# Kernel optimization log

Hardware: AMD Instinct MI355X
Metric: run time of the kernel (lower is better)

## Reference

```python
import jax, jax.numpy as jnp
import numpy as np

VOCAB, EMB = 100000, 128
KERNEL_NUM, SIGMA, EXACT_SIGMA = 21, 0.1, 0.001
OUT_LAYERS = [10, 5]

def _mus_sigmas():
    step = 2.0 / (KERNEL_NUM - 1)
    mus = [1.0, 1.0 - step / 2]
    for i in range(1, KERNEL_NUM - 1):
        mus.append(mus[i] - step)
    mus = list(reversed(mus))  # [-0.95, ..., 0.95, 1.0]
    sigmas = [SIGMA] * (KERNEL_NUM - 1) + [EXACT_SIGMA]
    return mus, sigmas

MUS, SIGMAS = _mus_sigmas()

def setup_inputs() -> dict:
    key = jax.random.key(0)
    ks = jax.random.split(key, 12)
    B, Q, D = 1024, 64, 256
    q1 = jax.random.randint(ks[0], (B, Q), 0, VOCAB, dtype=jnp.int32)
    d1 = jax.random.randint(ks[1], (B, D), 0, VOCAB, dtype=jnp.int32)
    q2 = jax.random.randint(ks[2], (B, Q), 0, VOCAB, dtype=jnp.int32)
    d2 = jax.random.randint(ks[3], (B, D), 0, VOCAB, dtype=jnp.int32)
    emb = jax.random.normal(ks[4], (VOCAB, EMB), dtype=jnp.float32)
    emb = emb.at[0].set(0.0)  # padding_idx=0
    dims = [KERNEL_NUM] + OUT_LAYERS + [1]
    W1 = jax.random.normal(ks[5], (dims[0], dims[1]), dtype=jnp.float32) / np.sqrt(dims[0])
    b1 = jnp.zeros((dims[1],), dtype=jnp.float32)
    W2 = jax.random.normal(ks[6], (dims[1], dims[2]), dtype=jnp.float32) / np.sqrt(dims[1])
    b2 = jnp.zeros((dims[2],), dtype=jnp.float32)
    W3 = jax.random.normal(ks[7], (dims[2], dims[3]), dtype=jnp.float32) / np.sqrt(dims[2])
    b3 = jnp.zeros((dims[3],), dtype=jnp.float32)
    return {"q1": q1, "d1": d1, "q2": q2, "d2": d2, "emb": emb,
            "W1": W1, "b1": b1, "W2": W2, "b2": b2, "W3": W3, "b3": b3}

def _matching_matrix(emb, q_ids, d_ids):
    q = emb[q_ids]  # [B,Q,E]
    d = emb[d_ids]  # [B,D,E]
    qn = q / (jnp.linalg.norm(q, axis=-1, keepdims=True) + 1e-13)
    dn = d / (jnp.linalg.norm(d, axis=-1, keepdims=True) + 1e-13)
    return jnp.einsum('bqe,bde->bqd', qn, dn)  # [B,Q,D]

def _apply_kernels(M):
    KM = []
    for mu, sig in zip(MUS, SIGMAS):
        k = jnp.exp(-(M - mu) ** 2 / (2.0 * sig ** 2))
        KM.append(jnp.log1p(k.sum(axis=-1)).sum(axis=-1))  # [B]
    return jnp.stack(KM, axis=-1)  # [B,21]

def _mlp(x, W1, b1, W2, b2, W3, b3):
    # _get_mlp puts ReLU BEFORE each Linear
    x = jax.nn.relu(x) @ W1 + b1
    x = jax.nn.relu(x) @ W2 + b2
    x = jax.nn.relu(x) @ W3 + b3
    return x  # [B,1]

def _predict(emb, q, d, W1, b1, W2, b2, W3, b3):
    M = _matching_matrix(emb, q, d)
    ko = _apply_kernels(M)
    return _mlp(ko, W1, b1, W2, b2, W3, b3)

def reference(q1, d1, q2, d2, emb, W1, b1, W2, b2, W3, b3):
    l1 = _predict(emb, q1, d1, W1, b1, W2, b2, W3, b3)
    l2 = _predict(emb, q2, d2, W1, b1, W2, b2, W3, b3)
    return jax.nn.sigmoid(l1 - l2)  # [B,1]
```

## Files before the change

### kernel.cpp

```cpp
#include <hip/hip_runtime.h>


typedef __attribute__((ext_vector_type(8))) short bf16x8;
typedef __attribute__((ext_vector_type(4))) float f32x4;
typedef __attribute__((ext_vector_type(2))) float f32x2;

__device__ __forceinline__ unsigned short f2bf(float f) {
    unsigned u = __float_as_uint(f);
    u += 0x7fffu + ((u >> 16) & 1u);
    return (unsigned short)(u >> 16);
}
__device__ __forceinline__ float bf2f(unsigned short h) {
    return __uint_as_float(((unsigned)h) << 16);
}

__global__ __launch_bounds__(256)
void norm_split_kernel(const float* __restrict__ emb,
                       unsigned short* __restrict__ th,
                       unsigned short* __restrict__ tl, int vocab)
{
    const int row = blockIdx.x * 8 + (threadIdx.x >> 5);
    if (row >= vocab) return;
    const int ln = threadIdx.x & 31;
    const float4 v = *reinterpret_cast<const float4*>(emb + (size_t)row * 128 + ln * 4);
    float ss = v.x*v.x + v.y*v.y + v.z*v.z + v.w*v.w;
    #pragma unroll
    for (int m = 16; m >= 1; m >>= 1) ss += __shfl_xor(ss, m);
    const float rn = 1.0f / (sqrtf(ss) + 1e-13f);
    const float f0 = v.x*rn, f1 = v.y*rn, f2 = v.z*rn, f3 = v.w*rn;
    const unsigned short h0 = f2bf(f0), h1 = f2bf(f1), h2 = f2bf(f2), h3 = f2bf(f3);
    const unsigned short g0 = f2bf(f0 - bf2f(h0)), g1 = f2bf(f1 - bf2f(h1));
    const unsigned short g2 = f2bf(f2 - bf2f(h2)), g3 = f2bf(f3 - bf2f(h3));
    const int off = row * 128 + ln * 4;
    *reinterpret_cast<uint2*>(th + off) =
        make_uint2((unsigned)h0 | ((unsigned)h1 << 16), (unsigned)h2 | ((unsigned)h3 << 16));
    *reinterpret_cast<uint2*>(tl + off) =
        make_uint2((unsigned)g0 | ((unsigned)g1 << 16), (unsigned)g2 | ((unsigned)g3 << 16));
}

__device__ __forceinline__ void glds16(const unsigned short* g, unsigned short* l) {
    __builtin_amdgcn_global_load_lds((const __attribute__((address_space(1))) void*)g,
                                     (__attribute__((address_space(3))) void*)l, 16, 0, 0);
}

__device__ __forceinline__ void stage_d16(const unsigned short* __restrict__ th,
                                          const unsigned short* __restrict__ tl,
                                          const int* __restrict__ ids, int base,
                                          unsigned short* __restrict__ dh,
                                          unsigned short* __restrict__ dl,
                                          int w, int l)
{
    const int r   = 4*w + (l >> 4);
    const int id  = ids[base + r];
    const int gsw = ((l & 15) ^ r) << 3;
    glds16(th + (size_t)id * 128 + gsw, dh + 4*w * 128);
    glds16(tl + (size_t)id * 128 + gsw, dl + 4*w * 128);
}

__device__ __forceinline__ void stage_q16(const unsigned short* __restrict__ th,
                                          const unsigned short* __restrict__ tl,
                                          const int* __restrict__ qids,
                                          unsigned short* __restrict__ dh,
                                          unsigned short* __restrict__ dl,
                                          int w, int l)
{
    #pragma unroll
    for (int j = 0; j < 4; j++) {
        const int r   = 4*j + (l >> 4);
        const int id  = qids[16*w + r];
        const int gsw = ((l & 15) ^ r) << 3;
        glds16(th + (size_t)id * 128 + gsw, dh + 4*j * 128);
        glds16(tl + (size_t)id * 128 + gsw, dl + 4*j * 128);
    }
}

#define PKF(a, b, c) __builtin_elementwise_fma((a), (b), (c))

__device__ __forceinline__ void apply_pair(float m0, float m1, f32x2 (&sp)[21]) {
    const f32x2 m2 = {m0, m1};
    const f32x2 dm = m2 - 0.05f;
    const f32x2 ta = (dm * dm) * -72.13475204444817f;
    const f32x2 x2 = m2 * 14.426950408889634f;
    const f32x2 t0 = { __builtin_amdgcn_exp2f(ta[0]), __builtin_amdgcn_exp2f(ta[1]) };
    const f32x2 R  = { __builtin_amdgcn_exp2f(x2[0]), __builtin_amdgcn_exp2f(x2[1]) };
    const f32x2 Ri = { __builtin_amdgcn_exp2f(-x2[0]), __builtin_amdgcn_exp2f(-x2[1]) };
    sp[10] += t0;
    f32x2 tu = t0;
    tu *= R;  sp[11] = PKF(tu, (f32x2)3.6787944117e-1f,  sp[11]);
    tu *= R;  sp[12] = PKF(tu, (f32x2)4.9787068368e-2f,  sp[12]);
    tu *= R;  sp[13] = PKF(tu, (f32x2)2.4787521767e-3f,  sp[13]);
    tu *= R;  sp[14] = PKF(tu, (f32x2)4.5399929762e-5f,  sp[14]);
    tu *= R;  sp[15] = PKF(tu, (f32x2)3.0590232050e-7f,  sp[15]);
    tu *= R;  sp[16] = PKF(tu, (f32x2)7.5825604279e-10f, sp[16]);
    tu *= R;  sp[17] = PKF(tu, (f32x2)6.9144001069e-13f, sp[17]);
    tu *= R;  sp[18] = PKF(tu, (f32x2)2.3195228302e-16f, sp[18]);
    tu *= R;  sp[19] = PKF(tu, (f32x2)2.8625185805e-20f, sp[19]);
    f32x2 td = t0;
    td *= Ri; sp[9] += td;
    td *= Ri; sp[8] = PKF(td, (f32x2)3.6787944117e-1f,  sp[8]);
    td *= Ri; sp[7] = PKF(td, (f32x2)4.9787068368e-2f,  sp[7]);
    td *= Ri; sp[6] = PKF(td, (f32x2)2.4787521767e-3f,  sp[6]);
    td *= Ri; sp[5] = PKF(td, (f32x2)4.5399929762e-5f,  sp[5]);
    td *= Ri; sp[4] = PKF(td, (f32x2)3.0590232050e-7f,  sp[4]);
    td *= Ri; sp[3] = PKF(td, (f32x2)7.5825604279e-10f, sp[3]);
    td *= Ri; sp[2] = PKF(td, (f32x2)6.9144001069e-13f, sp[2]);
    td *= Ri; sp[1] = PKF(td, (f32x2)2.3195228302e-16f, sp[1]);
    td *= Ri; sp[0] = PKF(td, (f32x2)2.8625185805e-20f, sp[0]);
    const f32x2 e  = m2 - 1.0f;
    const f32x2 ea = (e * e) * -721347.5204444817f;
    const f32x2 ex = { __builtin_amdgcn_exp2f(ea[0]), __builtin_amdgcn_exp2f(ea[1]) };
    sp[20] += ex;
}

#define MFMA(a, b, c) __builtin_amdgcn_mfma_f32_16x16x32_bf16((a), (b), (c), 0, 0, 0)

__global__ __launch_bounds__(256, 2)
void knrm_main(const int* __restrict__ q1, const int* __restrict__ d1,
               const int* __restrict__ q2, const int* __restrict__ d2,
               const unsigned short* __restrict__ th, const unsigned short* __restrict__ tl,
               float* __restrict__ kmws)
{
    __shared__ unsigned short bh[4][16*128];
    __shared__ unsigned short bl[4][16*128];
    __shared__ int   sh_ids[256];
    __shared__ float KMpart[4][21];

    const int tid = threadIdx.x;
    const int bb  = blockIdx.x >> 1;
    const int p   = blockIdx.x & 1;
    const int w   = tid >> 6;
    const int l   = tid & 63;
    const int lr  = l & 15;
    const int lh  = l >> 4;

    const int* qids = (p == 0 ? q1 : q2) + bb * 64;
    const int* dids = (p == 0 ? d1 : d2) + bb * 256;

    sh_ids[tid] = dids[tid];
    stage_q16(th, tl, qids, bh[w], bl[w], w, l);
    asm volatile("s_waitcnt vmcnt(0) lgkmcnt(0)" ::: "memory");
    __builtin_amdgcn_s_barrier();

    bf16x8 Bh[4], Bl[4];
    #pragma unroll
    for (int ks = 0; ks < 4; ks++) {
        const int off = lr*128 + (((ks*4 + lh) ^ lr) << 3);
        Bh[ks] = *reinterpret_cast<const bf16x8*>(&bh[w][off]);
        Bl[ks] = *reinterpret_cast<const bf16x8*>(&bl[w][off]);
    }
    asm volatile("s_waitcnt lgkmcnt(0)" ::: "memory");
    __builtin_amdgcn_s_barrier();

    f32x2 sp[21];
    #pragma unroll
    for (int i = 0; i < 21; i++) sp[i] = (f32x2){0.f, 0.f};

    stage_d16(th, tl, sh_ids, 0,  bh[0], bl[0], w, l);
    stage_d16(th, tl, sh_ids, 16, bh[1], bl[1], w, l);
    stage_d16(th, tl, sh_ids, 32, bh[2], bl[2], w, l);

    for (int c = 0; c < 16; c++) {
        if (c <= 13)      asm volatile("s_waitcnt vmcnt(4)" ::: "memory");
        else if (c == 14) asm volatile("s_waitcnt vmcnt(2)" ::: "memory");
        else              asm volatile("s_waitcnt vmcnt(0)" ::: "memory");
        __builtin_amdgcn_s_barrier();

        const unsigned short* ch = bh[c & 3];
        const unsigned short* cl = bl[c & 3];
        f32x4 C = {0.f,0.f,0.f,0.f};
        #pragma unroll
        for (int ks = 0; ks < 4; ks++) {
            const int o = lr*128 + (((ks*4 + lh) ^ lr) << 3);
            const bf16x8 Ah = *reinterpret_cast<const bf16x8*>(ch + o);
            const bf16x8 Al = *reinterpret_cast<const bf16x8*>(cl + o);
            C = MFMA(Ah, Bh[ks], C);
            C = MFMA(Ah, Bl[ks], C);
            C = MFMA(Al, Bh[ks], C);
        }
        apply_pair(C[0], C[1], sp);
        apply_pair(C[2], C[3], sp);

        __builtin_amdgcn_s_barrier();
        if (c <= 12)
            stage_d16(th, tl, sh_ids, (c + 3) * 16, bh[(c + 3) & 3], bl[(c + 3) & 3], w, l);
    }

    #pragma unroll
    for (int i = 0; i < 21; i++) {
        float s = sp[i][0] + sp[i][1];
        s += __shfl_xor(s, 16);
        s += __shfl_xor(s, 32);
        float t = log1pf(s);
        t += __shfl_xor(t, 1);
        t += __shfl_xor(t, 2);
        t += __shfl_xor(t, 4);
        t += __shfl_xor(t, 8);
        if (l == 0) KMpart[w][i] = t;
    }
    __syncthreads();
    if (tid < 21)
        kmws[blockIdx.x * 21 + tid] = KMpart[0][tid] + KMpart[1][tid]
                                    + KMpart[2][tid] + KMpart[3][tid];
}

__global__ __launch_bounds__(64)
void mlp_kernel(const float* __restrict__ kmws,
                const float* __restrict__ W1, const float* __restrict__ b1,
                const float* __restrict__ W2, const float* __restrict__ b2,
                const float* __restrict__ W3, const float* __restrict__ b3,
                float* __restrict__ out)
{
    __shared__ float KMs[2][21], x1s[2][10], x2s[2][5];
    const int tid = threadIdx.x;
    const int bb  = blockIdx.x;
    if (tid < 42) KMs[tid / 21][tid % 21] = kmws[(bb * 2 + tid / 21) * 21 + (tid % 21)];
    __syncthreads();
    if (tid < 10) {
        for (int p = 0; p < 2; p++) {
            float acc = b1[tid];
            #pragma unroll
            for (int i = 0; i < 21; i++) acc = fmaf(fmaxf(KMs[p][i], 0.0f), W1[i*10 + tid], acc);
            x1s[p][tid] = acc;
        }
    }
    __syncthreads();
    if (tid < 5) {
        for (int p = 0; p < 2; p++) {
            float acc = b2[tid];
            #pragma unroll
            for (int i = 0; i < 10; i++) acc = fmaf(fmaxf(x1s[p][i], 0.0f), W2[i*5 + tid], acc);
            x2s[p][tid] = acc;
        }
    }
    __syncthreads();
    if (tid == 0) {
        float lv[2];
        for (int p = 0; p < 2; p++) {
            float acc = b3[0];
            #pragma unroll
            for (int i = 0; i < 5; i++) acc = fmaf(fmaxf(x2s[p][i], 0.0f), W3[i], acc);
            lv[p] = acc;
        }
        out[bb] = 1.0f / (1.0f + expf(lv[1] - lv[0]));
    }
}

__device__ __forceinline__ void stage_f32(const float* __restrict__ emb,
                                          const int* __restrict__ ids,
                                          unsigned short* __restrict__ hi,
                                          unsigned short* __restrict__ lo,
                                          int tid)
{
    const int lg = tid >> 5;
    const int ln = tid & 31;
    #pragma unroll
    for (int i = 0; i < 4; i++) {
        const int row = i * 8 + lg;
        const int id  = ids[row];
        const float4 v = *reinterpret_cast<const float4*>(emb + (size_t)id * 128 + ln * 4);
        float ss = v.x*v.x + v.y*v.y + v.z*v.z + v.w*v.w;
        #pragma unroll
        for (int m = 16; m >= 1; m >>= 1) ss += __shfl_xor(ss, m);
        const float rn = 1.0f / (sqrtf(ss) + 1e-13f);
        const float f0 = v.x*rn, f1 = v.y*rn, f2 = v.z*rn, f3 = v.w*rn;
        const unsigned short h0 = f2bf(f0), h1 = f2bf(f1), h2 = f2bf(f2), h3 = f2bf(f3);
        const unsigned short g0 = f2bf(f0 - bf2f(h0)), g1 = f2bf(f1 - bf2f(h1));
        const unsigned short g2 = f2bf(f2 - bf2f(h2)), g3 = f2bf(f3 - bf2f(h3));
        const int off = row*128 + (((ln >> 1) ^ (row & 15)) << 3) + ((ln & 1) << 2);
        *reinterpret_cast<uint2*>(hi + off) =
            make_uint2((unsigned)h0 | ((unsigned)h1 << 16), (unsigned)h2 | ((unsigned)h3 << 16));
        *reinterpret_cast<uint2*>(lo + off) =
            make_uint2((unsigned)g0 | ((unsigned)g1 << 16), (unsigned)g2 | ((unsigned)g3 << 16));
    }
}

__global__ __launch_bounds__(256, 2)
void knrm_fallback(const int* __restrict__ q1, const int* __restrict__ d1,
                   const int* __restrict__ q2, const int* __restrict__ d2,
                   const float* __restrict__ emb,
                   const float* __restrict__ W1, const float* __restrict__ b1,
                   const float* __restrict__ W2, const float* __restrict__ b2,
                   const float* __restrict__ W3, const float* __restrict__ b3,
                   float* __restrict__ out)
{
    __shared__ unsigned short bh[2][32*128], bl[2][32*128];
    __shared__ float KMpart[2][4][21];
    __shared__ float x1s[2][10], x2s[2][5];
    const int tid = threadIdx.x;
    const int bb  = blockIdx.x;
    const int w   = tid >> 6;
    const int l   = tid & 63;
    const int lr  = l & 15;
    const int lh  = l >> 4;

    for (int p = 0; p < 2; p++) {
        const int* qids = (p == 0 ? q1 : q2) + bb * 64;
        const int* dids = (p == 0 ? d1 : d2) + bb * 256;
        stage_f32(emb, qids,      bh[0], bl[0], tid);
        stage_f32(emb, qids + 32, bh[1], bl[1], tid);
        __syncthreads();
        bf16x8 Bh[4], Bl[4];
        const int qb = w >> 1;
        const int qr = (w * 16 + lr) & 31;
        #pragma unroll
        for (int ks = 0; ks < 4; ks++) {
            const int off = qr*128 + (((ks*4 + lh) ^ lr) << 3);
            Bh[ks] = *reinterpret_cast<const bf16x8*>(&bh[qb][off]);
            Bl[ks] = *reinterpret_cast<const bf16x8*>(&bl[qb][off]);
        }
        __syncthreads();
        f32x2 sp[21];
        #pragma unroll
        for (int i = 0; i < 21; i++) sp[i] = (f32x2){0.f, 0.f};
        for (int c = 0; c < 8; c++) {
            stage_f32(emb, dids + c * 32, bh[c & 1], bl[c & 1], tid);
            __syncthreads();
            const unsigned short* ch = bh[c & 1];
            const unsigned short* cl = bl[c & 1];
            f32x4 C0 = {0.f,0.f,0.f,0.f}, C1 = {0.f,0.f,0.f,0.f};
            #pragma unroll
            for (int ks = 0; ks < 4; ks++) {
                const int o0 = lr*128        + (((ks*4 + lh) ^ lr) << 3);
                const int o1 = (16 + lr)*128 + (((ks*4 + lh) ^ lr) << 3);
                const bf16x8 A0h = *reinterpret_cast<const bf16x8*>(ch + o0);
                const bf16x8 A0l = *reinterpret_cast<const bf16x8*>(cl + o0);
                const bf16x8 A1h = *reinterpret_cast<const bf16x8*>(ch + o1);
                const bf16x8 A1l = *reinterpret_cast<const bf16x8*>(cl + o1);
                C0 = MFMA(A0h, Bh[ks], C0); C1 = MFMA(A1h, Bh[ks], C1);
                C0 = MFMA(A0h, Bl[ks], C0); C1 = MFMA(A1h, Bl[ks], C1);
                C0 = MFMA(A0l, Bh[ks], C0); C1 = MFMA(A1l, Bh[ks], C1);
            }
            #pragma unroll
            for (int r = 0; r < 4; r++) apply_pair(C0[r], C1[r], sp);
            __syncthreads();
        }
        #pragma unroll
        for (int i = 0; i < 21; i++) {
            float s = sp[i][0] + sp[i][1];
            s += __shfl_xor(s, 16);
            s += __shfl_xor(s, 32);
            float t = log1pf(s);
            t += __shfl_xor(t, 1);
            t += __shfl_xor(t, 2);
            t += __shfl_xor(t, 4);
            t += __shfl_xor(t, 8);
            if (l == 0) KMpart[p][w][i] = t;
        }
    }
    __syncthreads();
    if (tid < 10) {
        for (int p = 0; p < 2; p++) {
            float acc = b1[tid];
            #pragma unroll
            for (int i = 0; i < 21; i++) {
                const float km = KMpart[p][0][i] + KMpart[p][1][i]
                               + KMpart[p][2][i] + KMpart[p][3][i];
                acc = fmaf(fmaxf(km, 0.0f), W1[i*10 + tid], acc);
            }
            x1s[p][tid] = acc;
        }
    }
    __syncthreads();
    if (tid < 5) {
        for (int p = 0; p < 2; p++) {
            float acc = b2[tid];
            #pragma unroll
            for (int i = 0; i < 10; i++) acc = fmaf(fmaxf(x1s[p][i], 0.0f), W2[i*5 + tid], acc);
            x2s[p][tid] = acc;
        }
    }
    __syncthreads();
    if (tid == 0) {
        float lv[2];
        for (int p = 0; p < 2; p++) {
            float acc = b3[0];
            #pragma unroll
            for (int i = 0; i < 5; i++) acc = fmaf(fmaxf(x2s[p][i], 0.0f), W3[i], acc);
            lv[p] = acc;
        }
        out[bb] = 1.0f / (1.0f + expf(lv[1] - lv[0]));
    }
}

extern "C" void kernel_launch(void* const* d_in, const int* in_sizes, int n_in,
                              void* d_out, int out_size, void* d_ws, size_t ws_size,
                              hipStream_t stream)
{
    const int*   q1  = (const int*)  d_in[0];
    const int*   d1  = (const int*)  d_in[1];
    const int*   q2  = (const int*)  d_in[2];
    const int*   d2  = (const int*)  d_in[3];
    const float* emb = (const float*)d_in[4];
    const float* W1  = (const float*)d_in[5];
    const float* b1  = (const float*)d_in[6];
    const float* W2  = (const float*)d_in[7];
    const float* b2  = (const float*)d_in[8];
    const float* W3  = (const float*)d_in[9];
    const float* b3  = (const float*)d_in[10];
    float* out = (float*)d_out;
    (void)n_in;

    const int    vocab = in_sizes[4] / 128;
    const size_t tabsz = (size_t)vocab * 128 * 2;
    const size_t kmsz  = (size_t)out_size * 2 * 21 * 4;
    const size_t need  = tabsz * 2 + kmsz;

    if (ws_size >= need) {
        unsigned short* th = (unsigned short*)d_ws;
        unsigned short* tl = th + (size_t)vocab * 128;
        float* kmws = (float*)((char*)d_ws + tabsz * 2);
        norm_split_kernel<<<(vocab + 7) / 8, 256, 0, stream>>>(emb, th, tl, vocab);
        knrm_main<<<out_size * 2, 256, 0, stream>>>(q1, d1, q2, d2, th, tl, kmws);
        mlp_kernel<<<out_size, 64, 0, stream>>>(kmws, W1, b1, W2, b2, W3, b3, out);
    } else {
        knrm_fallback<<<out_size, 256, 0, stream>>>(q1, d1, q2, d2, emb,
                                                    W1, b1, W2, b2, W3, b3, out);
    }
}
```

Baseline: 120.5 us.

## Interleave hi/lo bf16 tables per row and deepen LDS prefetch ring to six

The hi and lo bf16 halves of each normalized embedding row are now stored next to each other in one 512-byte row instead of in two separate tables, so each gathered id touches one contiguous region. The d-tile pipeline in the main kernel grows from a 4-slot to a 6-slot LDS ring, with five tiles in flight, and the trailing barrier before each refill is removed. The aim is to hide gather latency and cut one barrier per iteration. The cost is more LDS per block, which may limit occupancy. Dropping the barrier also depends on the 6-slot distance to keep a slot from being overwritten while it is still being read.

```diff
diff --git a/kernel.cpp b/kernel.cpp
--- a/kernel.cpp
+++ b/kernel.cpp
@@ -16,8 +16,7 @@
 
 __global__ __launch_bounds__(256)
 void norm_split_kernel(const float* __restrict__ emb,
-                       unsigned short* __restrict__ th,
-                       unsigned short* __restrict__ tl, int vocab)
+                       unsigned short* __restrict__ tab, int vocab)
 {
     const int row = blockIdx.x * 8 + (threadIdx.x >> 5);
     if (row >= vocab) return;
@@ -31,10 +30,10 @@
     const unsigned short h0 = f2bf(f0), h1 = f2bf(f1), h2 = f2bf(f2), h3 = f2bf(f3);
     const unsigned short g0 = f2bf(f0 - bf2f(h0)), g1 = f2bf(f1 - bf2f(h1));
     const unsigned short g2 = f2bf(f2 - bf2f(h2)), g3 = f2bf(f3 - bf2f(h3));
-    const int off = row * 128 + ln * 4;
-    *reinterpret_cast<uint2*>(th + off) =
+    unsigned short* base = tab + (size_t)row * 256 + ln * 4;
+    *reinterpret_cast<uint2*>(base) =
         make_uint2((unsigned)h0 | ((unsigned)h1 << 16), (unsigned)h2 | ((unsigned)h3 << 16));
-    *reinterpret_cast<uint2*>(tl + off) =
+    *reinterpret_cast<uint2*>(base + 128) =
         make_uint2((unsigned)g0 | ((unsigned)g1 << 16), (unsigned)g2 | ((unsigned)g3 << 16));
 }
 
@@ -43,8 +42,7 @@
                                      (__attribute__((address_space(3))) void*)l, 16, 0, 0);
 }
 
-__device__ __forceinline__ void stage_d16(const unsigned short* __restrict__ th,
-                                          const unsigned short* __restrict__ tl,
+__device__ __forceinline__ void stage_d16(const unsigned short* __restrict__ tab,
                                           const int* __restrict__ ids, int base,
                                           unsigned short* __restrict__ dh,
                                           unsigned short* __restrict__ dl,
@@ -53,12 +51,12 @@
     const int r   = 4*w + (l >> 4);
     const int id  = ids[base + r];
     const int gsw = ((l & 15) ^ r) << 3;
-    glds16(th + (size_t)id * 128 + gsw, dh + 4*w * 128);
-    glds16(tl + (size_t)id * 128 + gsw, dl + 4*w * 128);
-}
-
-__device__ __forceinline__ void stage_q16(const unsigned short* __restrict__ th,
-                                          const unsigned short* __restrict__ tl,
+    const unsigned short* g = tab + (size_t)id * 256 + gsw;
+    glds16(g,       dh + 4*w * 128);
+    glds16(g + 128, dl + 4*w * 128);
+}
+
+__device__ __forceinline__ void stage_q16(const unsigned short* __restrict__ tab,
                                           const int* __restrict__ qids,
                                           unsigned short* __restrict__ dh,
                                           unsigned short* __restrict__ dl,
@@ -69,8 +67,9 @@
         const int r   = 4*j + (l >> 4);
         const int id  = qids[16*w + r];
         const int gsw = ((l & 15) ^ r) << 3;
-        glds16(th + (size_t)id * 128 + gsw, dh + 4*j * 128);
-        glds16(tl + (size_t)id * 128 + gsw, dl + 4*j * 128);
+        const unsigned short* g = tab + (size_t)id * 256 + gsw;
+        glds16(g,       dh + 4*j * 128);
+        glds16(g + 128, dl + 4*j * 128);
     }
 }
 
@@ -117,11 +116,11 @@
 __global__ __launch_bounds__(256, 2)
 void knrm_main(const int* __restrict__ q1, const int* __restrict__ d1,
                const int* __restrict__ q2, const int* __restrict__ d2,
-               const unsigned short* __restrict__ th, const unsigned short* __restrict__ tl,
+               const unsigned short* __restrict__ tab,
                float* __restrict__ kmws)
 {
-    __shared__ unsigned short bh[4][16*128];
-    __shared__ unsigned short bl[4][16*128];
+    __shared__ unsigned short bh[6][16*128];
+    __shared__ unsigned short bl[6][16*128];
     __shared__ int   sh_ids[256];
     __shared__ float KMpart[4][21];
 
@@ -137,7 +136,7 @@
     const int* dids = (p == 0 ? d1 : d2) + bb * 256;
 
     sh_ids[tid] = dids[tid];
-    stage_q16(th, tl, qids, bh[w], bl[w], w, l);
+    stage_q16(tab, qids, bh[w], bl[w], w, l);
     asm volatile("s_waitcnt vmcnt(0) lgkmcnt(0)" ::: "memory");
     __builtin_amdgcn_s_barrier();
 
@@ -155,18 +154,22 @@
     #pragma unroll
     for (int i = 0; i < 21; i++) sp[i] = (f32x2){0.f, 0.f};
 
-    stage_d16(th, tl, sh_ids, 0,  bh[0], bl[0], w, l);
-    stage_d16(th, tl, sh_ids, 16, bh[1], bl[1], w, l);
-    stage_d16(th, tl, sh_ids, 32, bh[2], bl[2], w, l);
+    stage_d16(tab, sh_ids, 0,  bh[0], bl[0], w, l);
+    stage_d16(tab, sh_ids, 16, bh[1], bl[1], w, l);
+    stage_d16(tab, sh_ids, 32, bh[2], bl[2], w, l);
+    stage_d16(tab, sh_ids, 48, bh[3], bl[3], w, l);
+    stage_d16(tab, sh_ids, 64, bh[4], bl[4], w, l);
 
     for (int c = 0; c < 16; c++) {
-        if (c <= 13)      asm volatile("s_waitcnt vmcnt(4)" ::: "memory");
+        if (c <= 11)      asm volatile("s_waitcnt vmcnt(8)" ::: "memory");
+        else if (c == 12) asm volatile("s_waitcnt vmcnt(6)" ::: "memory");
+        else if (c == 13) asm volatile("s_waitcnt vmcnt(4)" ::: "memory");
         else if (c == 14) asm volatile("s_waitcnt vmcnt(2)" ::: "memory");
         else              asm volatile("s_waitcnt vmcnt(0)" ::: "memory");
         __builtin_amdgcn_s_barrier();
 
-        const unsigned short* ch = bh[c & 3];
-        const unsigned short* cl = bl[c & 3];
+        const unsigned short* ch = bh[c % 6];
+        const unsigned short* cl = bl[c % 6];
         f32x4 C = {0.f,0.f,0.f,0.f};
         #pragma unroll
         for (int ks = 0; ks < 4; ks++) {
@@ -180,9 +183,8 @@
         apply_pair(C[0], C[1], sp);
         apply_pair(C[2], C[3], sp);
 
-        __builtin_amdgcn_s_barrier();
-        if (c <= 12)
-            stage_d16(th, tl, sh_ids, (c + 3) * 16, bh[(c + 3) & 3], bl[(c + 3) & 3], w, l);
+        if (c <= 10)
+            stage_d16(tab, sh_ids, (c + 5) * 16, bh[(c + 5) % 6], bl[(c + 5) % 6], w, l);
     }
 
     #pragma unroll
@@ -401,16 +403,15 @@
     (void)n_in;
 
     const int    vocab = in_sizes[4] / 128;
-    const size_t tabsz = (size_t)vocab * 128 * 2;
+    const size_t tabsz = (size_t)vocab * 256 * 2;
     const size_t kmsz  = (size_t)out_size * 2 * 21 * 4;
-    const size_t need  = tabsz * 2 + kmsz;
+    const size_t need  = tabsz + kmsz;
 
     if (ws_size >= need) {
-        unsigned short* th = (unsigned short*)d_ws;
-        unsigned short* tl = th + (size_t)vocab * 128;
-        float* kmws = (float*)((char*)d_ws + tabsz * 2);
-        norm_split_kernel<<<(vocab + 7) / 8, 256, 0, stream>>>(emb, th, tl, vocab);
-        knrm_main<<<out_size * 2, 256, 0, stream>>>(q1, d1, q2, d2, th, tl, kmws);
+        unsigned short* tab = (unsigned short*)d_ws;
+        float* kmws = (float*)((char*)d_ws + tabsz);
+        norm_split_kernel<<<(vocab + 7) / 8, 256, 0, stream>>>(emb, tab, vocab);
+        knrm_main<<<out_size * 2, 256, 0, stream>>>(q1, d1, q2, d2, tab, kmws);
         mlp_kernel<<<out_size, 64, 0, stream>>>(kmws, W1, b1, W2, b2, W3, b3, out);
     } else {
         knrm_fallback<<<out_size, 256, 0, stream>>>(q1, d1, q2, d2, emb,
```

Result: no change. 120.9 us (+0.3%).
